# Optimization experiments

Measured on AMD Instinct MI355X. Metric: run time of the kernel, lower is better.

The kernel has to match this reference:

```python
import jax, jax.numpy as jnp
import numpy as np

B, N, C = 4, 1024, 256
E = 65536
HID = 256  # LAYERS = [256, 256, 256]

def _linear_init(key, out_dim, in_dim):
    kw, kb = jax.random.split(key)
    s = 1.0 / np.sqrt(in_dim)
    W = jax.random.uniform(kw, (out_dim, in_dim), jnp.float32, -s, s)
    b = jax.random.uniform(kb, (out_dim,), jnp.float32, -s, s)
    return W, b

def setup_inputs() -> dict:
    key = jax.random.key(0)
    ks = jax.random.split(key, 5)
    pooled_features = jax.random.normal(ks[0], (B, N, C), jnp.float32)
    edge_index = jax.random.randint(ks[1], (2, E), 0, B * N)  # [src; dst]
    W1, b1 = _linear_init(ks[2], HID, 2 * C)
    W2, b2 = _linear_init(ks[3], HID, 2 * HID)
    W3, b3 = _linear_init(ks[4], HID, 2 * HID)
    return {"pooled_features": pooled_features, "edge_index": edge_index,
            "W1": W1, "b1": b1, "W2": W2, "b2": b2, "W3": W3, "b3": b3}

def _edge_conv(x, src, dst, num_nodes, W, b):
    # PyG EdgeConv: x_j = x[src], x_i = x[dst]; msg = relu(fc([x_j - x_i, x_i]));
    # aggr='max' scatters messages onto dst nodes.
    x_i = x[dst]                                   # [E, d]
    x_j = x[src]                                   # [E, d]
    msg = jnp.concatenate([x_j - x_i, x_i], axis=-1)  # [E, 2d]
    msg = jax.nn.relu(msg @ W.T + b)               # [E, out]
    out = jax.ops.segment_max(msg, dst, num_segments=num_nodes)
    # empty segments -> -inf; PyG fills with 0, and relu messages are >= 0
    return jnp.maximum(out, 0.0)

def reference(pooled_features, edge_index, W1, b1, W2, b2, W3, b3):
    b_, n_, c_ = pooled_features.shape
    num_nodes = b_ * n_
    x = pooled_features.reshape(num_nodes, c_)
    src, dst = edge_index[0], edge_index[1]
    feats = [x]
    for W, bb in ((W1, b1), (W2, b2), (W3, b3)):
        x = _edge_conv(x, src, dst, num_nodes, W, bb)
        feats.append(x)
    related_features = jnp.concatenate(feats, axis=-1)  # [num_nodes, 1024]
    return related_features
```

## Files before the change

kernel.cpp:

```cpp
#include <hip/hip_runtime.h>
#include <hip/hip_bf16.h>


#define NODES 4096
#define EDGES 65536
#define OSTR 1024

typedef __attribute__((ext_vector_type(8))) short bf16x8;
typedef __attribute__((ext_vector_type(4))) float f32x4;

__device__ __forceinline__ unsigned short f2bf(float f) {
    unsigned int x = __float_as_uint(f);
    return (unsigned short)((x + 0x7fff + ((x >> 16) & 1)) >> 16);
}
__device__ __forceinline__ float bf2f(unsigned short u) {
    return __uint_as_float(((unsigned int)u) << 16);
}

__global__ __launch_bounds__(256) void k_setup(const float* __restrict__ x0,
                                               float* __restrict__ out,
                                               unsigned short* __restrict__ xbuf,
                                               const float* __restrict__ W0,
                                               const float* __restrict__ W1,
                                               const float* __restrict__ W2,
                                               short* __restrict__ Wp,
                                               int* __restrict__ cnt) {
    int b = blockIdx.x, t = threadIdx.x;
    if (b < NODES) {
        int idx = b * 256 + t;
        float v = x0[idx];
        out[b * OSTR + (idx & 255)] = v;
        xbuf[idx] = f2bf(v);
    } else if (b < NODES + 1536) {
        int b2 = b - NODES;
        int layer = b2 >> 9;
        int idx = (b2 & 511) * 256 + t;
        const float* W = layer == 0 ? W0 : (layer == 1 ? W1 : W2);
        int n = idx >> 8, c = idx & 255;
        float v;
        if (n < 256) v = W[n * 512 + c];
        else         v = W[(n - 256) * 512 + 256 + c] - W[(n - 256) * 512 + c];
        Wp[layer * 131072 + idx] = (short)f2bf(v);
    } else {
        cnt[(b - NODES - 1536) * 256 + t] = 0;
    }
}

__global__ __launch_bounds__(256) void k_hist(const int* __restrict__ dst,
                                              int* __restrict__ cnt) {
    int e = blockIdx.x * 256 + threadIdx.x;
    atomicAdd(&cnt[dst[e]], 1);
}
__global__ __launch_bounds__(256) void k_scan(int* __restrict__ cnt,
                                              int* __restrict__ offsets) {
    __shared__ int part[256];
    int t = threadIdx.x, base = t * 16;
    int loc[16], s = 0;
#pragma unroll
    for (int j = 0; j < 16; ++j) { loc[j] = cnt[base + j]; s += loc[j]; }
    part[t] = s;
    __syncthreads();
    for (int d = 1; d < 256; d <<= 1) {
        int v = (t >= d) ? part[t - d] : 0;
        __syncthreads();
        part[t] += v;
        __syncthreads();
    }
    int run = part[t] - s;
#pragma unroll
    for (int j = 0; j < 16; ++j) { offsets[base + j] = run; run += loc[j]; cnt[base + j] = 0; }
    if (t == 255) offsets[4096] = run;
}
__global__ __launch_bounds__(256) void k_scatter(const int* __restrict__ src,
                                                 const int* __restrict__ dst,
                                                 const int* __restrict__ offsets,
                                                 int* __restrict__ cursor,
                                                 int* __restrict__ srcS) {
    int e = blockIdx.x * 256 + threadIdx.x;
    int d = dst[e];
    int p = offsets[d] + atomicAdd(&cursor[d], 1);
    srcS[p] = src[e];
}

__global__ __launch_bounds__(256) void k_gemm(const unsigned short* __restrict__ xbuf,
                                              const short* __restrict__ Wp,
                                              const float* __restrict__ bias,
                                              unsigned short* __restrict__ UWu,
                                              float* __restrict__ UWw) {
    __shared__ __align__(16) short Alds[32 * 264];

    const int t = threadIdx.x;
    const int m0 = blockIdx.x * 32;
    const int nhalf = blockIdx.y;

    {
        int r = t >> 3, ch = t & 7;
        const int4* ps = (const int4*)(xbuf + (size_t)(m0 + r) * 256);
        short* arow = &Alds[r * 264];
#pragma unroll
        for (int j = 0; j < 4; ++j) {
            int c = ch + 8 * j;
            *(int4*)(arow + c * 8) = ps[c];
        }
    }
    __syncthreads();

    const int wave = t >> 6, lane = t & 63;
    const int lm = lane & 15, kq = lane >> 4;
    const int nbl = wave * 64;
    const int nb = nhalf * 256 + nbl;

    f32x4 acc[2][4];
#pragma unroll
    for (int mt = 0; mt < 2; ++mt)
#pragma unroll
        for (int nt = 0; nt < 4; ++nt) acc[mt][nt] = (f32x4){0.f, 0.f, 0.f, 0.f};

    const short* a0p = &Alds[lm * 264 + kq * 8];
    const short* a1p = a0p + 16 * 264;
    const short* bp = Wp + (size_t)(nb + lm) * 256 + kq * 8;

#pragma unroll
    for (int ks = 0; ks < 8; ++ks) {
        const int ko = ks * 32;
        bf16x8 a0 = *(const bf16x8*)(a0p + ko);
        bf16x8 a1 = *(const bf16x8*)(a1p + ko);
        bf16x8 b0 = *(const bf16x8*)(bp + ko);
        bf16x8 b1 = *(const bf16x8*)(bp + 16 * 256 + ko);
        bf16x8 b2 = *(const bf16x8*)(bp + 32 * 256 + ko);
        bf16x8 b3 = *(const bf16x8*)(bp + 48 * 256 + ko);
        acc[0][0] = __builtin_amdgcn_mfma_f32_16x16x32_bf16(a0, b0, acc[0][0], 0, 0, 0);
        acc[0][1] = __builtin_amdgcn_mfma_f32_16x16x32_bf16(a0, b1, acc[0][1], 0, 0, 0);
        acc[0][2] = __builtin_amdgcn_mfma_f32_16x16x32_bf16(a0, b2, acc[0][2], 0, 0, 0);
        acc[0][3] = __builtin_amdgcn_mfma_f32_16x16x32_bf16(a0, b3, acc[0][3], 0, 0, 0);
        acc[1][0] = __builtin_amdgcn_mfma_f32_16x16x32_bf16(a1, b0, acc[1][0], 0, 0, 0);
        acc[1][1] = __builtin_amdgcn_mfma_f32_16x16x32_bf16(a1, b1, acc[1][1], 0, 0, 0);
        acc[1][2] = __builtin_amdgcn_mfma_f32_16x16x32_bf16(a1, b2, acc[1][2], 0, 0, 0);
        acc[1][3] = __builtin_amdgcn_mfma_f32_16x16x32_bf16(a1, b3, acc[1][3], 0, 0, 0);
    }

#pragma unroll
    for (int nt = 0; nt < 4; ++nt) {
        int nc = nbl + nt * 16 + lm;
        float bc = (nhalf == 1) ? bias[nc] : 0.0f;
#pragma unroll
        for (int mt = 0; mt < 2; ++mt) {
#pragma unroll
            for (int p = 0; p < 4; ++p) {
                int erow = mt * 16 + kq * 4 + p;
                float v = acc[mt][nt][p] + bc;
                size_t off = (size_t)(m0 + erow) * 256 + nc;
                if (nhalf == 0) UWu[off] = f2bf(v);
                else            UWw[off] = v;
            }
        }
    }
}

__global__ __launch_bounds__(256) void k_edge(const unsigned short* __restrict__ UWu,
                                              const float* __restrict__ UWw,
                                              const int* __restrict__ offsets,
                                              const int* __restrict__ srcS,
                                              float* __restrict__ out,
                                              unsigned short* __restrict__ xbuf,
                                              int ooff) {
    const int i = blockIdx.x * 4 + (threadIdx.x >> 6);
    const int l = threadIdx.x & 63;
    const int beg = offsets[i], end = offsets[i + 1];

    const float NEG = -3.4e38f;
    float m0 = NEG, m1 = NEG, m2 = NEG, m3 = NEG;
    int e = beg;
    for (; e + 4 <= end; e += 4) {
        int s0 = srcS[e], s1 = srcS[e + 1], s2 = srcS[e + 2], s3 = srcS[e + 3];
        ushort4 v0 = *(const ushort4*)(UWu + (size_t)s0 * 256 + l * 4);
        ushort4 v1 = *(const ushort4*)(UWu + (size_t)s1 * 256 + l * 4);
        ushort4 v2 = *(const ushort4*)(UWu + (size_t)s2 * 256 + l * 4);
        ushort4 v3 = *(const ushort4*)(UWu + (size_t)s3 * 256 + l * 4);
        m0 = fmaxf(fmaxf(fmaxf(m0, bf2f(v0.x)), fmaxf(bf2f(v1.x), bf2f(v2.x))), bf2f(v3.x));
        m1 = fmaxf(fmaxf(fmaxf(m1, bf2f(v0.y)), fmaxf(bf2f(v1.y), bf2f(v2.y))), bf2f(v3.y));
        m2 = fmaxf(fmaxf(fmaxf(m2, bf2f(v0.z)), fmaxf(bf2f(v1.z), bf2f(v2.z))), bf2f(v3.z));
        m3 = fmaxf(fmaxf(fmaxf(m3, bf2f(v0.w)), fmaxf(bf2f(v1.w), bf2f(v2.w))), bf2f(v3.w));
    }
    for (; e < end; ++e) {
        int s = srcS[e];
        ushort4 v = *(const ushort4*)(UWu + (size_t)s * 256 + l * 4);
        m0 = fmaxf(m0, bf2f(v.x)); m1 = fmaxf(m1, bf2f(v.y));
        m2 = fmaxf(m2, bf2f(v.z)); m3 = fmaxf(m3, bf2f(v.w));
    }
    float4 w = *(const float4*)(UWw + (size_t)i * 256 + l * 4);
    float4 r;
    r.x = fmaxf(m0 + w.x, 0.0f);
    r.y = fmaxf(m1 + w.y, 0.0f);
    r.z = fmaxf(m2 + w.z, 0.0f);
    r.w = fmaxf(m3 + w.w, 0.0f);
    *(float4*)(out + (size_t)i * OSTR + ooff + l * 4) = r;
    ushort4 rb;
    rb.x = f2bf(r.x); rb.y = f2bf(r.y); rb.z = f2bf(r.z); rb.w = f2bf(r.w);
    *(ushort4*)(xbuf + (size_t)i * 256 + l * 4) = rb;
}

extern "C" void kernel_launch(void* const* d_in, const int* in_sizes, int n_in,
                              void* d_out, int out_size, void* d_ws, size_t ws_size,
                              hipStream_t stream) {
    const float* x0 = (const float*)d_in[0];
    const int* ei = (const int*)d_in[1];
    const int* srcIdx = ei;
    const int* dstIdx = ei + EDGES;
    float* out = (float*)d_out;

    char* w = (char*)d_ws;
    unsigned short* UWu = (unsigned short*)w;
    float* UWw = (float*)(w + 2097152);
    unsigned short* xbuf = (unsigned short*)(w + 6291456);
    short* Wp = (short*)(w + 8388608);
    int* offsets = (int*)(w + 9175040);
    int* cnt = (int*)(w + 9191552);
    int* srcS = (int*)(w + 9207936);

    k_setup<<<NODES + 1536 + 16, 256, 0, stream>>>(x0, out, xbuf,
                                                   (const float*)d_in[2], (const float*)d_in[4],
                                                   (const float*)d_in[6], Wp, cnt);
    k_hist<<<EDGES / 256, 256, 0, stream>>>(dstIdx, cnt);
    k_scan<<<1, 256, 0, stream>>>(cnt, offsets);
    k_scatter<<<EDGES / 256, 256, 0, stream>>>(srcIdx, dstIdx, offsets, cnt, srcS);

    for (int l = 0; l < 3; ++l) {
        k_gemm<<<dim3(NODES / 32, 2), 256, 0, stream>>>(xbuf, Wp + l * 131072,
                                                        (const float*)d_in[3 + 2 * l],
                                                        UWu, UWw);
        k_edge<<<NODES / 4, 256, 0, stream>>>(UWu, UWw, offsets, srcS, out, xbuf,
                                              (l + 1) * 256);
    }
}
```

Baseline: 146.4 us.

## Fuse all stages into one cooperative persistent kernel with grid syncs

Replaces ten separate launches (setup, histogram, scan, scatter, and three GEMM+edge pairs) with one cooperative kernel of 256 blocks of 512 threads, using grid.sync between phases. The goal is to remove per-launch overhead and inter-kernel gaps, which dominate because each stage is small. The edge max loop also gains an 8-way unrolled gather path. In exchange, only 256 blocks run, so per-phase parallelism and latency hiding drop. Grid-wide barriers add their own cost, and the scan phase runs on a single block while the rest wait.

```diff
diff --git a/kernel.cpp b/kernel.cpp
--- a/kernel.cpp
+++ b/kernel.cpp
@@ -1,5 +1,7 @@
 #include <hip/hip_runtime.h>
-#include <hip/hip_bf16.h>
+#include <hip/hip_cooperative_groups.h>
+
+namespace cg = cooperative_groups;
 
 
 #define NODES 4096
@@ -17,187 +19,200 @@
     return __uint_as_float(((unsigned int)u) << 16);
 }
 
-__global__ __launch_bounds__(256) void k_setup(const float* __restrict__ x0,
-                                               float* __restrict__ out,
-                                               unsigned short* __restrict__ xbuf,
-                                               const float* __restrict__ W0,
-                                               const float* __restrict__ W1,
-                                               const float* __restrict__ W2,
-                                               short* __restrict__ Wp,
-                                               int* __restrict__ cnt) {
-    int b = blockIdx.x, t = threadIdx.x;
-    if (b < NODES) {
-        int idx = b * 256 + t;
-        float v = x0[idx];
-        out[b * OSTR + (idx & 255)] = v;
-        xbuf[idx] = f2bf(v);
-    } else if (b < NODES + 1536) {
-        int b2 = b - NODES;
-        int layer = b2 >> 9;
-        int idx = (b2 & 511) * 256 + t;
-        const float* W = layer == 0 ? W0 : (layer == 1 ? W1 : W2);
-        int n = idx >> 8, c = idx & 255;
-        float v;
-        if (n < 256) v = W[n * 512 + c];
-        else         v = W[(n - 256) * 512 + 256 + c] - W[(n - 256) * 512 + c];
-        Wp[layer * 131072 + idx] = (short)f2bf(v);
-    } else {
-        cnt[(b - NODES - 1536) * 256 + t] = 0;
-    }
-}
-
-__global__ __launch_bounds__(256) void k_hist(const int* __restrict__ dst,
-                                              int* __restrict__ cnt) {
-    int e = blockIdx.x * 256 + threadIdx.x;
-    atomicAdd(&cnt[dst[e]], 1);
-}
-__global__ __launch_bounds__(256) void k_scan(int* __restrict__ cnt,
-                                              int* __restrict__ offsets) {
-    __shared__ int part[256];
-    int t = threadIdx.x, base = t * 16;
-    int loc[16], s = 0;
-#pragma unroll
-    for (int j = 0; j < 16; ++j) { loc[j] = cnt[base + j]; s += loc[j]; }
-    part[t] = s;
-    __syncthreads();
-    for (int d = 1; d < 256; d <<= 1) {
-        int v = (t >= d) ? part[t - d] : 0;
+__global__ __launch_bounds__(512, 2) void k_all(
+    const float* __restrict__ x0,
+    const int* __restrict__ srcIdx, const int* __restrict__ dstIdx,
+    const float* __restrict__ W0, const float* __restrict__ B0,
+    const float* __restrict__ W1, const float* __restrict__ B1,
+    const float* __restrict__ W2, const float* __restrict__ B2,
+    float* __restrict__ out,
+    unsigned short* __restrict__ UWu,
+    float* __restrict__ UWw,
+    unsigned short* __restrict__ xbuf,
+    short* __restrict__ Wp,
+    int* __restrict__ offsets,
+    int* __restrict__ cnt,
+    int* __restrict__ srcS)
+{
+    __shared__ __align__(16) short Alds[32 * 264];
+    cg::grid_group grid = cg::this_grid();
+    const int t = threadIdx.x;
+    const int b = blockIdx.x;
+    const int gtid = b * 512 + t;
+
+    {
+#pragma unroll
+        for (int j = 0; j < 2; ++j) {
+            int i4 = j * 131072 + gtid;
+            float4 v = ((const float4*)x0)[i4];
+            int n = i4 >> 6, c4 = i4 & 63;
+            ((float4*)out)[(size_t)n * 256 + c4] = v;
+            ushort4 hb;
+            hb.x = f2bf(v.x); hb.y = f2bf(v.y); hb.z = f2bf(v.z); hb.w = f2bf(v.w);
+            ((ushort4*)xbuf)[i4] = hb;
+        }
+        const float* Ws[3] = {W0, W1, W2};
+#pragma unroll
+        for (int j = 0; j < 3; ++j) {
+            int n = gtid >> 8, c = gtid & 255;
+            const float* W = Ws[j];
+            float v = (n < 256) ? W[n * 512 + c]
+                                : W[(n - 256) * 512 + 256 + c] - W[(n - 256) * 512 + c];
+            Wp[j * 131072 + gtid] = (short)f2bf(v);
+        }
+        if (gtid < NODES) cnt[gtid] = 0;
+    }
+    grid.sync();
+
+    if (gtid < EDGES) atomicAdd(&cnt[dstIdx[gtid]], 1);
+    grid.sync();
+
+    if (b == 0) {
+        int* part = (int*)Alds;
+        int loc[16], s = 0;
+        if (t < 256) {
+            int base = t * 16;
+#pragma unroll
+            for (int j = 0; j < 16; ++j) { loc[j] = cnt[base + j]; s += loc[j]; }
+            part[t] = s;
+        }
         __syncthreads();
-        part[t] += v;
+        for (int d = 1; d < 256; d <<= 1) {
+            int v = (t < 256 && t >= d) ? part[t - d] : 0;
+            __syncthreads();
+            if (t < 256) part[t] += v;
+            __syncthreads();
+        }
+        if (t < 256) {
+            int run = part[t] - s, base = t * 16;
+#pragma unroll
+            for (int j = 0; j < 16; ++j) { offsets[base + j] = run; run += loc[j]; cnt[base + j] = 0; }
+            if (t == 255) offsets[4096] = run;
+        }
+    }
+    grid.sync();
+
+    if (gtid < EDGES) {
+        int d = dstIdx[gtid];
+        int p = offsets[d] + atomicAdd(&cnt[d], 1);
+        srcS[p] = srcIdx[gtid];
+    }
+
+    const int wv = t >> 6, lane = t & 63;
+    const int lm = lane & 15, kq = lane >> 4;
+    const int M0 = (b & 127) * 32;
+    const int nhalf = b >> 7;
+    const int rh = wv >> 2, cgf = wv & 3;
+    const float* biases[3] = {B0, B1, B2};
+
+#pragma unroll
+    for (int l = 0; l < 3; ++l) {
+        const short* Wl = Wp + l * 131072;
+
+#pragma unroll
+        for (int j = 0; j < 2; ++j) {
+            int q = j * 512 + t;
+            int r = q >> 5, ch = q & 31;
+            *(int4*)(Alds + r * 264 + ch * 8) =
+                *(const int4*)(xbuf + (size_t)(M0 + r) * 256 + ch * 8);
+        }
         __syncthreads();
-    }
-    int run = part[t] - s;
-#pragma unroll
-    for (int j = 0; j < 16; ++j) { offsets[base + j] = run; run += loc[j]; cnt[base + j] = 0; }
-    if (t == 255) offsets[4096] = run;
-}
-__global__ __launch_bounds__(256) void k_scatter(const int* __restrict__ src,
-                                                 const int* __restrict__ dst,
-                                                 const int* __restrict__ offsets,
-                                                 int* __restrict__ cursor,
-                                                 int* __restrict__ srcS) {
-    int e = blockIdx.x * 256 + threadIdx.x;
-    int d = dst[e];
-    int p = offsets[d] + atomicAdd(&cursor[d], 1);
-    srcS[p] = src[e];
-}
-
-__global__ __launch_bounds__(256) void k_gemm(const unsigned short* __restrict__ xbuf,
-                                              const short* __restrict__ Wp,
-                                              const float* __restrict__ bias,
-                                              unsigned short* __restrict__ UWu,
-                                              float* __restrict__ UWw) {
-    __shared__ __align__(16) short Alds[32 * 264];
-
-    const int t = threadIdx.x;
-    const int m0 = blockIdx.x * 32;
-    const int nhalf = blockIdx.y;
-
-    {
-        int r = t >> 3, ch = t & 7;
-        const int4* ps = (const int4*)(xbuf + (size_t)(m0 + r) * 256);
-        short* arow = &Alds[r * 264];
-#pragma unroll
-        for (int j = 0; j < 4; ++j) {
-            int c = ch + 8 * j;
-            *(int4*)(arow + c * 8) = ps[c];
-        }
-    }
-    __syncthreads();
-
-    const int wave = t >> 6, lane = t & 63;
-    const int lm = lane & 15, kq = lane >> 4;
-    const int nbl = wave * 64;
-    const int nb = nhalf * 256 + nbl;
-
-    f32x4 acc[2][4];
-#pragma unroll
-    for (int mt = 0; mt < 2; ++mt)
-#pragma unroll
-        for (int nt = 0; nt < 4; ++nt) acc[mt][nt] = (f32x4){0.f, 0.f, 0.f, 0.f};
-
-    const short* a0p = &Alds[lm * 264 + kq * 8];
-    const short* a1p = a0p + 16 * 264;
-    const short* bp = Wp + (size_t)(nb + lm) * 256 + kq * 8;
-
-#pragma unroll
-    for (int ks = 0; ks < 8; ++ks) {
-        const int ko = ks * 32;
-        bf16x8 a0 = *(const bf16x8*)(a0p + ko);
-        bf16x8 a1 = *(const bf16x8*)(a1p + ko);
-        bf16x8 b0 = *(const bf16x8*)(bp + ko);
-        bf16x8 b1 = *(const bf16x8*)(bp + 16 * 256 + ko);
-        bf16x8 b2 = *(const bf16x8*)(bp + 32 * 256 + ko);
-        bf16x8 b3 = *(const bf16x8*)(bp + 48 * 256 + ko);
-        acc[0][0] = __builtin_amdgcn_mfma_f32_16x16x32_bf16(a0, b0, acc[0][0], 0, 0, 0);
-        acc[0][1] = __builtin_amdgcn_mfma_f32_16x16x32_bf16(a0, b1, acc[0][1], 0, 0, 0);
-        acc[0][2] = __builtin_amdgcn_mfma_f32_16x16x32_bf16(a0, b2, acc[0][2], 0, 0, 0);
-        acc[0][3] = __builtin_amdgcn_mfma_f32_16x16x32_bf16(a0, b3, acc[0][3], 0, 0, 0);
-        acc[1][0] = __builtin_amdgcn_mfma_f32_16x16x32_bf16(a1, b0, acc[1][0], 0, 0, 0);
-        acc[1][1] = __builtin_amdgcn_mfma_f32_16x16x32_bf16(a1, b1, acc[1][1], 0, 0, 0);
-        acc[1][2] = __builtin_amdgcn_mfma_f32_16x16x32_bf16(a1, b2, acc[1][2], 0, 0, 0);
-        acc[1][3] = __builtin_amdgcn_mfma_f32_16x16x32_bf16(a1, b3, acc[1][3], 0, 0, 0);
-    }
-
-#pragma unroll
-    for (int nt = 0; nt < 4; ++nt) {
-        int nc = nbl + nt * 16 + lm;
-        float bc = (nhalf == 1) ? bias[nc] : 0.0f;
-#pragma unroll
-        for (int mt = 0; mt < 2; ++mt) {
+
+        f32x4 acc[4];
+#pragma unroll
+        for (int nt = 0; nt < 4; ++nt) acc[nt] = (f32x4){0.f, 0.f, 0.f, 0.f};
+
+        const short* ap = &Alds[(rh * 16 + lm) * 264 + kq * 8];
+        const short* bp = Wl + (size_t)(nhalf * 256 + cgf * 64 + lm) * 256 + kq * 8;
+
+#pragma unroll
+        for (int ks = 0; ks < 8; ++ks) {
+            const int ko = ks * 32;
+            bf16x8 a  = *(const bf16x8*)(ap + ko);
+            bf16x8 q0 = *(const bf16x8*)(bp + ko);
+            bf16x8 q1 = *(const bf16x8*)(bp + 16 * 256 + ko);
+            bf16x8 q2 = *(const bf16x8*)(bp + 32 * 256 + ko);
+            bf16x8 q3 = *(const bf16x8*)(bp + 48 * 256 + ko);
+            acc[0] = __builtin_amdgcn_mfma_f32_16x16x32_bf16(a, q0, acc[0], 0, 0, 0);
+            acc[1] = __builtin_amdgcn_mfma_f32_16x16x32_bf16(a, q1, acc[1], 0, 0, 0);
+            acc[2] = __builtin_amdgcn_mfma_f32_16x16x32_bf16(a, q2, acc[2], 0, 0, 0);
+            acc[3] = __builtin_amdgcn_mfma_f32_16x16x32_bf16(a, q3, acc[3], 0, 0, 0);
+        }
+
+        const float* bias = biases[l];
+#pragma unroll
+        for (int nt = 0; nt < 4; ++nt) {
+            int nc = cgf * 64 + nt * 16 + lm;
+            float bc = (nhalf == 1) ? bias[nc] : 0.0f;
 #pragma unroll
             for (int p = 0; p < 4; ++p) {
-                int erow = mt * 16 + kq * 4 + p;
-                float v = acc[mt][nt][p] + bc;
-                size_t off = (size_t)(m0 + erow) * 256 + nc;
+                int erow = rh * 16 + kq * 4 + p;
+                float v = acc[nt][p] + bc;
+                size_t off = (size_t)(M0 + erow) * 256 + nc;
                 if (nhalf == 0) UWu[off] = f2bf(v);
                 else            UWw[off] = v;
             }
         }
-    }
-}
-
-__global__ __launch_bounds__(256) void k_edge(const unsigned short* __restrict__ UWu,
-                                              const float* __restrict__ UWw,
-                                              const int* __restrict__ offsets,
-                                              const int* __restrict__ srcS,
-                                              float* __restrict__ out,
-                                              unsigned short* __restrict__ xbuf,
-                                              int ooff) {
-    const int i = blockIdx.x * 4 + (threadIdx.x >> 6);
-    const int l = threadIdx.x & 63;
-    const int beg = offsets[i], end = offsets[i + 1];
-
-    const float NEG = -3.4e38f;
-    float m0 = NEG, m1 = NEG, m2 = NEG, m3 = NEG;
-    int e = beg;
-    for (; e + 4 <= end; e += 4) {
-        int s0 = srcS[e], s1 = srcS[e + 1], s2 = srcS[e + 2], s3 = srcS[e + 3];
-        ushort4 v0 = *(const ushort4*)(UWu + (size_t)s0 * 256 + l * 4);
-        ushort4 v1 = *(const ushort4*)(UWu + (size_t)s1 * 256 + l * 4);
-        ushort4 v2 = *(const ushort4*)(UWu + (size_t)s2 * 256 + l * 4);
-        ushort4 v3 = *(const ushort4*)(UWu + (size_t)s3 * 256 + l * 4);
-        m0 = fmaxf(fmaxf(fmaxf(m0, bf2f(v0.x)), fmaxf(bf2f(v1.x), bf2f(v2.x))), bf2f(v3.x));
-        m1 = fmaxf(fmaxf(fmaxf(m1, bf2f(v0.y)), fmaxf(bf2f(v1.y), bf2f(v2.y))), bf2f(v3.y));
-        m2 = fmaxf(fmaxf(fmaxf(m2, bf2f(v0.z)), fmaxf(bf2f(v1.z), bf2f(v2.z))), bf2f(v3.z));
-        m3 = fmaxf(fmaxf(fmaxf(m3, bf2f(v0.w)), fmaxf(bf2f(v1.w), bf2f(v2.w))), bf2f(v3.w));
-    }
-    for (; e < end; ++e) {
-        int s = srcS[e];
-        ushort4 v = *(const ushort4*)(UWu + (size_t)s * 256 + l * 4);
-        m0 = fmaxf(m0, bf2f(v.x)); m1 = fmaxf(m1, bf2f(v.y));
-        m2 = fmaxf(m2, bf2f(v.z)); m3 = fmaxf(m3, bf2f(v.w));
-    }
-    float4 w = *(const float4*)(UWw + (size_t)i * 256 + l * 4);
-    float4 r;
-    r.x = fmaxf(m0 + w.x, 0.0f);
-    r.y = fmaxf(m1 + w.y, 0.0f);
-    r.z = fmaxf(m2 + w.z, 0.0f);
-    r.w = fmaxf(m3 + w.w, 0.0f);
-    *(float4*)(out + (size_t)i * OSTR + ooff + l * 4) = r;
-    ushort4 rb;
-    rb.x = f2bf(r.x); rb.y = f2bf(r.y); rb.z = f2bf(r.z); rb.w = f2bf(r.w);
-    *(ushort4*)(xbuf + (size_t)i * 256 + l * 4) = rb;
+        grid.sync();
+
+        const int ooff = (l + 1) * 256;
+#pragma unroll
+        for (int rr = 0; rr < 2; ++rr) {
+            const int i = b * 16 + rr * 8 + wv;
+            const int beg = offsets[i], end = offsets[i + 1];
+            const float NEG = -3.4e38f;
+            float mx0 = NEG, mx1 = NEG, mx2 = NEG, mx3 = NEG;
+            int e = beg;
+            for (; e + 8 <= end; e += 8) {
+                int s0 = srcS[e + 0], s1 = srcS[e + 1], s2 = srcS[e + 2], s3 = srcS[e + 3];
+                int s4 = srcS[e + 4], s5 = srcS[e + 5], s6 = srcS[e + 6], s7 = srcS[e + 7];
+                ushort4 v0 = *(const ushort4*)(UWu + (size_t)s0 * 256 + lane * 4);
+                ushort4 v1 = *(const ushort4*)(UWu + (size_t)s1 * 256 + lane * 4);
+                ushort4 v2 = *(const ushort4*)(UWu + (size_t)s2 * 256 + lane * 4);
+                ushort4 v3 = *(const ushort4*)(UWu + (size_t)s3 * 256 + lane * 4);
+                ushort4 v4 = *(const ushort4*)(UWu + (size_t)s4 * 256 + lane * 4);
+                ushort4 v5 = *(const ushort4*)(UWu + (size_t)s5 * 256 + lane * 4);
+                ushort4 v6 = *(const ushort4*)(UWu + (size_t)s6 * 256 + lane * 4);
+                ushort4 v7 = *(const ushort4*)(UWu + (size_t)s7 * 256 + lane * 4);
+                mx0 = fmaxf(mx0, fmaxf(fmaxf(bf2f(v0.x), bf2f(v1.x)), fmaxf(bf2f(v2.x), bf2f(v3.x))));
+                mx0 = fmaxf(mx0, fmaxf(fmaxf(bf2f(v4.x), bf2f(v5.x)), fmaxf(bf2f(v6.x), bf2f(v7.x))));
+                mx1 = fmaxf(mx1, fmaxf(fmaxf(bf2f(v0.y), bf2f(v1.y)), fmaxf(bf2f(v2.y), bf2f(v3.y))));
+                mx1 = fmaxf(mx1, fmaxf(fmaxf(bf2f(v4.y), bf2f(v5.y)), fmaxf(bf2f(v6.y), bf2f(v7.y))));
+                mx2 = fmaxf(mx2, fmaxf(fmaxf(bf2f(v0.z), bf2f(v1.z)), fmaxf(bf2f(v2.z), bf2f(v3.z))));
+                mx2 = fmaxf(mx2, fmaxf(fmaxf(bf2f(v4.z), bf2f(v5.z)), fmaxf(bf2f(v6.z), bf2f(v7.z))));
+                mx3 = fmaxf(mx3, fmaxf(fmaxf(bf2f(v0.w), bf2f(v1.w)), fmaxf(bf2f(v2.w), bf2f(v3.w))));
+                mx3 = fmaxf(mx3, fmaxf(fmaxf(bf2f(v4.w), bf2f(v5.w)), fmaxf(bf2f(v6.w), bf2f(v7.w))));
+            }
+            for (; e + 4 <= end; e += 4) {
+                int s0 = srcS[e + 0], s1 = srcS[e + 1], s2 = srcS[e + 2], s3 = srcS[e + 3];
+                ushort4 v0 = *(const ushort4*)(UWu + (size_t)s0 * 256 + lane * 4);
+                ushort4 v1 = *(const ushort4*)(UWu + (size_t)s1 * 256 + lane * 4);
+                ushort4 v2 = *(const ushort4*)(UWu + (size_t)s2 * 256 + lane * 4);
+                ushort4 v3 = *(const ushort4*)(UWu + (size_t)s3 * 256 + lane * 4);
+                mx0 = fmaxf(mx0, fmaxf(fmaxf(bf2f(v0.x), bf2f(v1.x)), fmaxf(bf2f(v2.x), bf2f(v3.x))));
+                mx1 = fmaxf(mx1, fmaxf(fmaxf(bf2f(v0.y), bf2f(v1.y)), fmaxf(bf2f(v2.y), bf2f(v3.y))));
+                mx2 = fmaxf(mx2, fmaxf(fmaxf(bf2f(v0.z), bf2f(v1.z)), fmaxf(bf2f(v2.z), bf2f(v3.z))));
+                mx3 = fmaxf(mx3, fmaxf(fmaxf(bf2f(v0.w), bf2f(v1.w)), fmaxf(bf2f(v2.w), bf2f(v3.w))));
+            }
+            for (; e < end; ++e) {
+                int s = srcS[e];
+                ushort4 v = *(const ushort4*)(UWu + (size_t)s * 256 + lane * 4);
+                mx0 = fmaxf(mx0, bf2f(v.x)); mx1 = fmaxf(mx1, bf2f(v.y));
+                mx2 = fmaxf(mx2, bf2f(v.z)); mx3 = fmaxf(mx3, bf2f(v.w));
+            }
+            float4 w4 = *(const float4*)(UWw + (size_t)i * 256 + lane * 4);
+            float4 r;
+            r.x = fmaxf(mx0 + w4.x, 0.0f);
+            r.y = fmaxf(mx1 + w4.y, 0.0f);
+            r.z = fmaxf(mx2 + w4.z, 0.0f);
+            r.w = fmaxf(mx3 + w4.w, 0.0f);
+            *(float4*)(out + (size_t)i * OSTR + ooff + lane * 4) = r;
+            ushort4 rb;
+            rb.x = f2bf(r.x); rb.y = f2bf(r.y); rb.z = f2bf(r.z); rb.w = f2bf(r.w);
+            *(ushort4*)(xbuf + (size_t)i * 256 + lane * 4) = rb;
+        }
+        if (l < 2) grid.sync();
+    }
 }
 
 extern "C" void kernel_launch(void* const* d_in, const int* in_sizes, int n_in,
@@ -218,18 +233,14 @@
     int* cnt = (int*)(w + 9191552);
     int* srcS = (int*)(w + 9207936);
 
-    k_setup<<<NODES + 1536 + 16, 256, 0, stream>>>(x0, out, xbuf,
-                                                   (const float*)d_in[2], (const float*)d_in[4],
-                                                   (const float*)d_in[6], Wp, cnt);
-    k_hist<<<EDGES / 256, 256, 0, stream>>>(dstIdx, cnt);
-    k_scan<<<1, 256, 0, stream>>>(cnt, offsets);
-    k_scatter<<<EDGES / 256, 256, 0, stream>>>(srcIdx, dstIdx, offsets, cnt, srcS);
-
-    for (int l = 0; l < 3; ++l) {
-        k_gemm<<<dim3(NODES / 32, 2), 256, 0, stream>>>(xbuf, Wp + l * 131072,
-                                                        (const float*)d_in[3 + 2 * l],
-                                                        UWu, UWw);
-        k_edge<<<NODES / 4, 256, 0, stream>>>(UWu, UWw, offsets, srcS, out, xbuf,
-                                              (l + 1) * 256);
-    }
-}
+    const float* W0 = (const float*)d_in[2]; const float* B0 = (const float*)d_in[3];
+    const float* W1 = (const float*)d_in[4]; const float* B1 = (const float*)d_in[5];
+    const float* W2 = (const float*)d_in[6]; const float* B2 = (const float*)d_in[7];
+
+    void* args[] = {(void*)&x0, (void*)&srcIdx, (void*)&dstIdx,
+                    (void*)&W0, (void*)&B0, (void*)&W1, (void*)&B1,
+                    (void*)&W2, (void*)&B2,
+                    (void*)&out, (void*)&UWu, (void*)&UWw, (void*)&xbuf, (void*)&Wp,
+                    (void*)&offsets, (void*)&cnt, (void*)&srcS};
+    hipLaunchCooperativeKernel((void*)k_all, dim3(256), dim3(512), args, 0, stream);
+}
```

Result: slower. 391.3 us (+167.2%).
